# Optimization experiments

Measured on AMD Instinct MI355X. Metric: run time of the kernel, lower is better.

Reference implementation:

```python
import jax, jax.numpy as jnp
import numpy as np

N, S, F, D = 4096, 128, 128, 256  # batch, memory slots, feat_dim, dim_h_o
EPS = 1e-8  # torch CosineSimilarity eps


def _xavier(key, shape):
    fan_out, fan_in = shape
    std = float(np.sqrt(2.0 / (fan_in + fan_out)))
    return jax.random.normal(key, shape, dtype=jnp.float32) * std


def setup_inputs() -> dict:
    key = jax.random.key(0)
    ks = jax.random.split(key, 10)
    return {
        "h_o_prev": jax.random.normal(ks[0], (N, D), dtype=jnp.float32),
        "C": jax.random.normal(ks[1], (N, S, F), dtype=jnp.float32),
        "Wk": _xavier(ks[2], (F, D)), "bk": jnp.zeros((F,), jnp.float32),
        "Wb": _xavier(ks[3], (1, D)), "bb": jnp.zeros((1,), jnp.float32),
        "We": _xavier(ks[4], (F, D)), "be": jnp.zeros((F,), jnp.float32),
        "Wv": _xavier(ks[5], (F, D)), "bv": jnp.zeros((F,), jnp.float32),
        "Wih": _xavier(ks[6], (3 * D, F)), "Whh": _xavier(ks[7], (3 * D, D)),
        "bih": jnp.zeros((3 * D,), jnp.float32), "bhh": jnp.zeros((3 * D,), jnp.float32),
    }


def reference(h_o_prev, C, Wk, bk, Wb, bb, We, be, Wv, bv, Wih, Whh, bih, bhh):
    # --- Attention (content addressing) ---
    k = h_o_prev @ Wk.T + bk                              # [N, F]
    beta_pre = h_o_prev @ Wb.T + bb                       # [N, 1]
    # clamp-split softplus trick in source == softplus(x) + 1
    beta = jax.nn.softplus(beta_pre) + 1.0                # [N, 1]
    C_norm = jnp.maximum(jnp.linalg.norm(C, axis=2), EPS)           # [N, S]
    k_norm = jnp.maximum(jnp.linalg.norm(k, axis=1, keepdims=True), EPS)  # [N, 1]
    s = jnp.einsum("nsf,nf->ns", C, k) / (C_norm * k_norm)          # cosine sim [N, S]
    w = jax.nn.softmax(s * beta, axis=1)                  # [N, S]
    # --- Read memory ---
    r = jnp.einsum("ns,nsf->nf", w, C)                    # [N, F]
    # --- GRU cell update (torch GRUCell semantics) ---
    gi = r @ Wih.T + bih                                  # [N, 3D]
    gh = h_o_prev @ Whh.T + bhh                           # [N, 3D]
    i_r, i_z, i_n = jnp.split(gi, 3, axis=1)
    h_r, h_z, h_n = jnp.split(gh, 3, axis=1)
    rg = jax.nn.sigmoid(i_r + h_r)
    z = jax.nn.sigmoid(i_z + h_z)
    n = jnp.tanh(i_n + rg * h_n)
    h_o = (1.0 - z) * n + z * h_o_prev                    # [N, D]
    # --- Write memory (erase + add, outer products) ---
    e = jax.nn.sigmoid(h_o @ We.T + be)                   # [N, F]
    v = h_o @ Wv.T + bv                                   # [N, F]
    w2 = w[:, :, None]                                    # [N, S, 1]
    C_new = C * (1.0 - w2 * e[:, None, :]) + w2 * v[:, None, :]
    return h_o, C_new, k, r
```

## Files before the change

kernel.cpp:

```cpp
#include <hip/hip_runtime.h>
#include <hip/hip_bf16.h>
#include <cstddef>
#include <cstdint>

constexpr int Nn = 4096;
constexpr int Ss = 128;
constexpr int Ff = 128;
constexpr int Dd = 256;
constexpr float EPSV = 1e-8f;

constexpr size_t HO_OFF = 0;
constexpr size_t C_OFF  = (size_t)Nn * Dd;
constexpr size_t K_OFF  = C_OFF + (size_t)Nn * Ss * Ff;
constexpr size_t R_OFF  = K_OFF + (size_t)Nn * Ff;

typedef __attribute__((ext_vector_type(4))) float f4v;
typedef __attribute__((ext_vector_type(8))) short bh8;

__device__ __forceinline__ float sigmf(float x) { return 1.0f / (1.0f + __expf(-x)); }

__device__ __forceinline__ short f2bf(float x) {
    __hip_bfloat16 h = __float2bfloat16(x);
    return *reinterpret_cast<short*>(&h);
}

template <int SIGSPLIT>
__global__ __launch_bounds__(256) void mfma_gemm(
    const float* __restrict__ A, int K,
    const float* __restrict__ W1, const float* __restrict__ W2, int splitW,
    const float* __restrict__ b1, const float* __restrict__ b2,
    float* __restrict__ out1, int J1,
    float* __restrict__ out2, int J2, int splitOut)
{
    __shared__ __align__(16) short sA[64 * 32];
    __shared__ __align__(16) short sW[64 * 32];

    const int t  = threadIdx.x;
    const int bm = blockIdx.x * 64;
    const int bj = blockIdx.y * 64;

    const int r  = t >> 2;
    const int kg = t & 3;
    const float* aRow = A + (size_t)(bm + r) * K;
    const int   colS  = bj + r;
    const float* wRow = (colS < splitW) ? (W1 + (size_t)colS * K)
                                        : (W2 + (size_t)(colS - splitW) * K);
    const int swzSt = r * 32 + ((kg ^ (r & 3)) << 3);

    const int l   = t & 63;
    const int wv  = t >> 6;
    const int wr  = wv >> 1;
    const int wc  = wv & 1;
    const int kgr = l >> 4;
    const int fr  = l & 15;

    f4v acc[2][2];
#pragma unroll
    for (int m = 0; m < 2; ++m)
#pragma unroll
        for (int n2 = 0; n2 < 2; ++n2) acc[m][n2] = f4v{0.f, 0.f, 0.f, 0.f};

    const int nk = K / 32;
    for (int kc = 0; kc < nk; ++kc) {
        const int k0 = kc * 32 + kg * 8;
        float4 a0 = *(const float4*)(aRow + k0);
        float4 a1 = *(const float4*)(aRow + k0 + 4);
        float4 w0 = *(const float4*)(wRow + k0);
        float4 w1 = *(const float4*)(wRow + k0 + 4);
        bh8 av = { f2bf(a0.x), f2bf(a0.y), f2bf(a0.z), f2bf(a0.w),
                   f2bf(a1.x), f2bf(a1.y), f2bf(a1.z), f2bf(a1.w) };
        bh8 wvv= { f2bf(w0.x), f2bf(w0.y), f2bf(w0.z), f2bf(w0.w),
                   f2bf(w1.x), f2bf(w1.y), f2bf(w1.z), f2bf(w1.w) };
        __syncthreads();
        *(bh8*)(sA + swzSt) = av;
        *(bh8*)(sW + swzSt) = wvv;
        __syncthreads();

        bh8 af[2], bf[2];
#pragma unroll
        for (int m = 0; m < 2; ++m) {
            int ar = wr * 32 + m * 16 + fr;
            af[m] = *(bh8*)(sA + ar * 32 + ((kgr ^ (ar & 3)) << 3));
            int bc = wc * 32 + m * 16 + fr;
            bf[m] = *(bh8*)(sW + bc * 32 + ((kgr ^ (bc & 3)) << 3));
        }
#pragma unroll
        for (int m = 0; m < 2; ++m)
#pragma unroll
            for (int n2 = 0; n2 < 2; ++n2)
                acc[m][n2] = __builtin_amdgcn_mfma_f32_16x16x32_bf16(
                    af[m], bf[n2], acc[m][n2], 0, 0, 0);
    }

#pragma unroll
    for (int n2 = 0; n2 < 2; ++n2) {
        const int colg = bj + wc * 32 + n2 * 16 + fr;
        const float bs = (colg < splitW) ? b1[colg] : b2[colg - splitW];
        float* base; int jj;
        if (colg < splitOut) { base = out1 + colg;              jj = J1; }
        else                 { base = out2 + (colg - splitOut); jj = J2; }
#pragma unroll
        for (int m = 0; m < 2; ++m) {
#pragma unroll
            for (int rg = 0; rg < 4; ++rg) {
                float x = acc[m][n2][rg] + bs;
                if (SIGSPLIT && colg < SIGSPLIT) x = sigmf(x);
                const int rowg = bm + wr * 32 + m * 16 + kgr * 4 + rg;
                base[(size_t)rowg * jj] = x;
            }
        }
    }
}

__global__ __launch_bounds__(256) void beta_kernel(
    const float* __restrict__ h, const float* __restrict__ Wb,
    const float* __restrict__ bb, float* __restrict__ beta_out)
{
    int wid  = threadIdx.x >> 6;
    int lane = threadIdx.x & 63;
    int n    = blockIdx.x * 4 + wid;
    float4 hv = *(const float4*)(h + (size_t)n * Dd + lane * 4);
    float4 wv = *(const float4*)(Wb + lane * 4);
    float p = hv.x * wv.x + hv.y * wv.y + hv.z * wv.z + hv.w * wv.w;
#pragma unroll
    for (int o = 32; o > 0; o >>= 1) p += __shfl_xor(p, o);
    if (lane == 0) {
        float bp = p + bb[0];
        float sp = (bp > 20.0f) ? bp : log1pf(__expf(bp));
        beta_out[n] = sp + 1.0f;
    }
}

__global__ __launch_bounds__(256) void attn_kernel(
    const float* __restrict__ C, const float* __restrict__ kvec,
    const float* __restrict__ beta_arr,
    float* __restrict__ w_out, float* __restrict__ r_out)
{
    const int n    = blockIdx.x;
    const int t    = threadIdx.x;
    const int lane = t & 63;
    const int wid  = t >> 6;
    const float* Cn = C + (size_t)n * Ss * Ff;

    __shared__ float sk[Ff];
    __shared__ float ssc[Ss];
    __shared__ float sred[8];
    __shared__ float sw[Ss];
    __shared__ float sr4[8][Ff];

    if (t < Ff) sk[t] = kvec[(size_t)n * Ff + t];
    __syncthreads();

    float ks = 0.0f;
    if (t < Ff) { float kv = sk[t]; ks = kv * kv; }
#pragma unroll
    for (int o = 32; o > 0; o >>= 1) ks += __shfl_xor(ks, o);
    if (lane == 0) sred[wid] = ks;
    __syncthreads();
    const float knorm = fmaxf(sqrtf(sred[0] + sred[1]), EPSV);
    const float beta  = beta_arr[n];

#pragma unroll 4
    for (int it = 0; it < 16; ++it) {
        int s = wid * 32 + it * 2 + (lane >> 5);
        int f = (lane & 31) * 4;
        float4 c4 = *(const float4*)(Cn + (size_t)s * Ff + f);
        float d = c4.x * sk[f] + c4.y * sk[f + 1] + c4.z * sk[f + 2] + c4.w * sk[f + 3];
        float q = c4.x * c4.x + c4.y * c4.y + c4.z * c4.z + c4.w * c4.w;
#pragma unroll
        for (int o = 16; o > 0; o >>= 1) {
            d += __shfl_xor(d, o);
            q += __shfl_xor(q, o);
        }
        if ((lane & 31) == 0) {
            float cn = fmaxf(sqrtf(q), EPSV);
            ssc[s] = d / (cn * knorm);
        }
    }
    __syncthreads();

    float x = -INFINITY;
    if (t < Ss) x = ssc[t] * beta;
    float m = x;
#pragma unroll
    for (int o = 32; o > 0; o >>= 1) m = fmaxf(m, __shfl_xor(m, o));
    if (lane == 0) sred[wid] = m;
    __syncthreads();
    const float gm = fmaxf(sred[0], sred[1]);
    float ex = (t < Ss) ? __expf(x - gm) : 0.0f;
    float sm = ex;
#pragma unroll
    for (int o = 32; o > 0; o >>= 1) sm += __shfl_xor(sm, o);
    if (lane == 0) sred[4 + wid] = sm;
    __syncthreads();
    const float tot = sred[4] + sred[5];
    if (t < Ss) {
        float wvl = ex / tot;
        sw[t] = wvl;
        w_out[(size_t)n * Ss + t] = wvl;
    }
    __syncthreads();

    const int f4 = (t & 31) * 4;
    const int sg = t >> 5;
    float4 racc = make_float4(0.f, 0.f, 0.f, 0.f);
#pragma unroll 4
    for (int j = 0; j < 16; ++j) {
        int s = sg * 16 + j;
        float wvl = sw[s];
        float4 c4 = *(const float4*)(Cn + (size_t)s * Ff + f4);
        racc.x += wvl * c4.x;
        racc.y += wvl * c4.y;
        racc.z += wvl * c4.z;
        racc.w += wvl * c4.w;
    }
    *(float4*)(&sr4[sg][f4]) = racc;
    __syncthreads();
    if (t < 32) {
        float4 rr = *(float4*)(&sr4[0][t * 4]);
#pragma unroll
        for (int g = 1; g < 8; ++g) {
            float4 p = *(float4*)(&sr4[g][t * 4]);
            rr.x += p.x; rr.y += p.y; rr.z += p.z; rr.w += p.w;
        }
        *(float4*)(r_out + (size_t)n * Ff + t * 4) = rr;
    }
}

__global__ __launch_bounds__(256) void gates_kernel(
    const float* __restrict__ gi, const float* __restrict__ gh,
    const float* __restrict__ hprev, float* __restrict__ ho)
{
    int idx = blockIdx.x * blockDim.x + threadIdx.x;
    int n  = idx >> 6;
    int d4 = (idx & 63) * 4;
    const float* gin = gi + (size_t)n * 768;
    const float* ghn = gh + (size_t)n * 768;
    float4 ir = *(const float4*)(gin + d4);
    float4 iz = *(const float4*)(gin + 256 + d4);
    float4 in_ = *(const float4*)(gin + 512 + d4);
    float4 hr = *(const float4*)(ghn + d4);
    float4 hz = *(const float4*)(ghn + 256 + d4);
    float4 hn = *(const float4*)(ghn + 512 + d4);
    float4 hp = *(const float4*)(hprev + (size_t)n * Dd + d4);
    float4 o;
    { float rg = sigmf(ir.x + hr.x); float z = sigmf(iz.x + hz.x);
      float nn = tanhf(in_.x + rg * hn.x); o.x = (1.0f - z) * nn + z * hp.x; }
    { float rg = sigmf(ir.y + hr.y); float z = sigmf(iz.y + hz.y);
      float nn = tanhf(in_.y + rg * hn.y); o.y = (1.0f - z) * nn + z * hp.y; }
    { float rg = sigmf(ir.z + hr.z); float z = sigmf(iz.z + hz.z);
      float nn = tanhf(in_.z + rg * hn.z); o.z = (1.0f - z) * nn + z * hp.z; }
    { float rg = sigmf(ir.w + hr.w); float z = sigmf(iz.w + hz.w);
      float nn = tanhf(in_.w + rg * hn.w); o.w = (1.0f - z) * nn + z * hp.w; }
    *(float4*)(ho + (size_t)n * Dd + d4) = o;
}

__global__ __launch_bounds__(256) void update_kernel(
    const float* __restrict__ C, const float* __restrict__ w,
    const float* __restrict__ ev, float* __restrict__ Cnew)
{
    const size_t total4 = (size_t)Nn * Ss * Ff / 4;
    const size_t stride = (size_t)gridDim.x * blockDim.x;
    const size_t lin    = (size_t)blockIdx.x * blockDim.x + threadIdx.x;
    const int nIter     = (int)(total4 / stride);
    for (int it = nIter - 1; it >= 0; --it) {
        size_t i = (size_t)it * stride + lin;
        int n   = (int)(i >> 12);
        int rem = (int)(i & 4095);
        int s   = rem >> 5;
        int f4  = (rem & 31) * 4;
        float wv = w[(size_t)n * Ss + s];
        float4 e4 = *(const float4*)(ev + (size_t)n * 256 + f4);
        float4 v4 = *(const float4*)(ev + (size_t)n * 256 + 128 + f4);
        f4v c4 = __builtin_nontemporal_load((const f4v*)(C + i * 4));
        f4v o;
        o.x = c4.x * (1.0f - wv * e4.x) + wv * v4.x;
        o.y = c4.y * (1.0f - wv * e4.y) + wv * v4.y;
        o.z = c4.z * (1.0f - wv * e4.z) + wv * v4.z;
        o.w = c4.w * (1.0f - wv * e4.w) + wv * v4.w;
        __builtin_nontemporal_store(o, (f4v*)(Cnew + i * 4));
    }
}

extern "C" void kernel_launch(void* const* d_in, const int* in_sizes, int n_in,
                              void* d_out, int out_size, void* d_ws, size_t ws_size,
                              hipStream_t stream)
{
    const float* h_prev = (const float*)d_in[0];
    const float* C      = (const float*)d_in[1];
    const float* Wk     = (const float*)d_in[2];
    const float* bk     = (const float*)d_in[3];
    const float* Wb     = (const float*)d_in[4];
    const float* bb     = (const float*)d_in[5];
    const float* We     = (const float*)d_in[6];
    const float* be     = (const float*)d_in[7];
    const float* Wv     = (const float*)d_in[8];
    const float* bv     = (const float*)d_in[9];
    const float* Wih    = (const float*)d_in[10];
    const float* Whh    = (const float*)d_in[11];
    const float* bih    = (const float*)d_in[12];
    const float* bhh    = (const float*)d_in[13];

    float* out  = (float*)d_out;
    float* ho   = out + HO_OFF;
    float* Cnew = out + C_OFF;
    float* kbuf = out + K_OFF;
    float* rbuf = out + R_OFF;

    float* ws      = (float*)d_ws;
    float* ws_gh   = ws;
    float* ws_gi   = ws_gh + (size_t)Nn * 768;
    float* ws_beta = ws_gi + (size_t)Nn * 768;
    float* ws_w    = ws_beta + Nn;
    float* ws_ev   = ws_w + (size_t)Nn * Ss;

    mfma_gemm<0><<<dim3(Nn / 64, 896 / 64), 256, 0, stream>>>(
        h_prev, Dd, Whh, Wk, 768, bhh, bk, ws_gh, 768, kbuf, 128, 768);

    beta_kernel<<<Nn / 4, 256, 0, stream>>>(h_prev, Wb, bb, ws_beta);

    attn_kernel<<<Nn, 256, 0, stream>>>(C, kbuf, ws_beta, ws_w, rbuf);

    mfma_gemm<0><<<dim3(Nn / 64, 768 / 64), 256, 0, stream>>>(
        rbuf, Ff, Wih, Wih, 768, bih, bih, ws_gi, 768, nullptr, 0, 768);

    gates_kernel<<<(Nn * Dd / 4) / 256, 256, 0, stream>>>(ws_gi, ws_gh, h_prev, ho);

    mfma_gemm<128><<<dim3(Nn / 64, 256 / 64), 256, 0, stream>>>(
        ho, Dd, We, Wv, 128, be, bv, ws_ev, 256, nullptr, 0, 256);

    update_kernel<<<8192, 256, 0, stream>>>(C, ws_w, ws_ev, Cnew);
}
```

Measured before the change: 227.8 us.

## Fuse key/beta projections into attention, cache C in LDS as bf16, batch GRU GEMMs

The k projection and the beta softplus are now computed inside the attention kernel, one block per row, each thread dotting a Wk row against h in shared memory. This removes the separate beta kernel and the k round-trip through global memory. The attention kernel also stores C as bf16 in LDS so the weighted read pass no longer re-reads C from global memory, at the cost of bf16 rounding in r and higher LDS use that may lower occupancy. The h·Whh and r·Wih GEMMs are merged into one launch using a z-dimension, and the GEMM loops register-prefetch the next K tile.

```diff
diff --git a/kernel.cpp b/kernel.cpp
--- a/kernel.cpp
+++ b/kernel.cpp
@@ -16,6 +16,7 @@
 
 typedef __attribute__((ext_vector_type(4))) float f4v;
 typedef __attribute__((ext_vector_type(8))) short bh8;
+typedef __attribute__((ext_vector_type(4))) short bh4;
 
 __device__ __forceinline__ float sigmf(float x) { return 1.0f / (1.0f + __expf(-x)); }
 
@@ -23,17 +24,23 @@
     __hip_bfloat16 h = __float2bfloat16(x);
     return *reinterpret_cast<short*>(&h);
 }
-
-template <int SIGSPLIT>
-__global__ __launch_bounds__(256) void mfma_gemm(
-    const float* __restrict__ A, int K,
-    const float* __restrict__ W1, const float* __restrict__ W2, int splitW,
-    const float* __restrict__ b1, const float* __restrict__ b2,
-    float* __restrict__ out1, int J1,
-    float* __restrict__ out2, int J2, int splitOut)
+__device__ __forceinline__ float bf2f(short s) {
+    return __uint_as_float(((unsigned int)(unsigned short)s) << 16);
+}
+
+
+__global__ __launch_bounds__(256) void gemm_dual(
+    const float* __restrict__ A0, int K0, const float* __restrict__ W0,
+    const float* __restrict__ bias0, float* __restrict__ out0,
+    const float* __restrict__ A1, int K1, const float* __restrict__ W1,
+    const float* __restrict__ bias1, float* __restrict__ out1, int J)
 {
     __shared__ __align__(16) short sA[64 * 32];
     __shared__ __align__(16) short sW[64 * 32];
+
+    const float* A;  const float* W;  const float* bias;  float* out;  int K;
+    if (blockIdx.z == 0) { A = A0; W = W0; bias = bias0; out = out0; K = K0; }
+    else                 { A = A1; W = W1; bias = bias1; out = out1; K = K1; }
 
     const int t  = threadIdx.x;
     const int bm = blockIdx.x * 64;
@@ -42,9 +49,7 @@
     const int r  = t >> 2;
     const int kg = t & 3;
     const float* aRow = A + (size_t)(bm + r) * K;
-    const int   colS  = bj + r;
-    const float* wRow = (colS < splitW) ? (W1 + (size_t)colS * K)
-                                        : (W2 + (size_t)(colS - splitW) * K);
+    const float* wRow = W + (size_t)(bj + r) * K;
     const int swzSt = r * 32 + ((kg ^ (r & 3)) << 3);
 
     const int l   = t & 63;
@@ -61,21 +66,27 @@
         for (int n2 = 0; n2 < 2; ++n2) acc[m][n2] = f4v{0.f, 0.f, 0.f, 0.f};
 
     const int nk = K / 32;
+    float4 a0 = *(const float4*)(aRow + kg * 8);
+    float4 a1 = *(const float4*)(aRow + kg * 8 + 4);
+    float4 w0 = *(const float4*)(wRow + kg * 8);
+    float4 w1 = *(const float4*)(wRow + kg * 8 + 4);
+
     for (int kc = 0; kc < nk; ++kc) {
-        const int k0 = kc * 32 + kg * 8;
-        float4 a0 = *(const float4*)(aRow + k0);
-        float4 a1 = *(const float4*)(aRow + k0 + 4);
-        float4 w0 = *(const float4*)(wRow + k0);
-        float4 w1 = *(const float4*)(wRow + k0 + 4);
         bh8 av = { f2bf(a0.x), f2bf(a0.y), f2bf(a0.z), f2bf(a0.w),
                    f2bf(a1.x), f2bf(a1.y), f2bf(a1.z), f2bf(a1.w) };
-        bh8 wvv= { f2bf(w0.x), f2bf(w0.y), f2bf(w0.z), f2bf(w0.w),
+        bh8 wv8= { f2bf(w0.x), f2bf(w0.y), f2bf(w0.z), f2bf(w0.w),
                    f2bf(w1.x), f2bf(w1.y), f2bf(w1.z), f2bf(w1.w) };
         __syncthreads();
         *(bh8*)(sA + swzSt) = av;
-        *(bh8*)(sW + swzSt) = wvv;
+        *(bh8*)(sW + swzSt) = wv8;
         __syncthreads();
-
+        if (kc + 1 < nk) {
+            const int k0 = (kc + 1) * 32 + kg * 8;
+            a0 = *(const float4*)(aRow + k0);
+            a1 = *(const float4*)(aRow + k0 + 4);
+            w0 = *(const float4*)(wRow + k0);
+            w1 = *(const float4*)(wRow + k0 + 4);
+        }
         bh8 af[2], bf[2];
 #pragma unroll
         for (int m = 0; m < 2; ++m) {
@@ -95,46 +106,111 @@
 #pragma unroll
     for (int n2 = 0; n2 < 2; ++n2) {
         const int colg = bj + wc * 32 + n2 * 16 + fr;
-        const float bs = (colg < splitW) ? b1[colg] : b2[colg - splitW];
-        float* base; int jj;
-        if (colg < splitOut) { base = out1 + colg;              jj = J1; }
-        else                 { base = out2 + (colg - splitOut); jj = J2; }
+        const float bs = bias[colg];
+#pragma unroll
+        for (int m = 0; m < 2; ++m)
+#pragma unroll
+            for (int rg = 0; rg < 4; ++rg) {
+                const int rowg = bm + wr * 32 + m * 16 + kgr * 4 + rg;
+                out[(size_t)rowg * J + colg] = acc[m][n2][rg] + bs;
+            }
+    }
+}
+
+__global__ __launch_bounds__(256) void gemm_ev(
+    const float* __restrict__ A,
+    const float* __restrict__ We, const float* __restrict__ Wv,
+    const float* __restrict__ be, const float* __restrict__ bv,
+    float* __restrict__ out)
+{
+    constexpr int K = 256, J = 256;
+    __shared__ __align__(16) short sA[64 * 32];
+    __shared__ __align__(16) short sW[64 * 32];
+
+    const int t  = threadIdx.x;
+    const int bm = blockIdx.x * 64;
+    const int bj = blockIdx.y * 64;
+
+    const int r  = t >> 2;
+    const int kg = t & 3;
+    const float* aRow = A + (size_t)(bm + r) * K;
+    const int colS = bj + r;
+    const float* wRow = (colS < 128) ? (We + (size_t)colS * K)
+                                     : (Wv + (size_t)(colS - 128) * K);
+    const int swzSt = r * 32 + ((kg ^ (r & 3)) << 3);
+
+    const int l   = t & 63;
+    const int wv  = t >> 6;
+    const int wr  = wv >> 1;
+    const int wc  = wv & 1;
+    const int kgr = l >> 4;
+    const int fr  = l & 15;
+
+    f4v acc[2][2];
+#pragma unroll
+    for (int m = 0; m < 2; ++m)
+#pragma unroll
+        for (int n2 = 0; n2 < 2; ++n2) acc[m][n2] = f4v{0.f, 0.f, 0.f, 0.f};
+
+    const int nk = K / 32;
+    float4 a0 = *(const float4*)(aRow + kg * 8);
+    float4 a1 = *(const float4*)(aRow + kg * 8 + 4);
+    float4 w0 = *(const float4*)(wRow + kg * 8);
+    float4 w1 = *(const float4*)(wRow + kg * 8 + 4);
+
+    for (int kc = 0; kc < nk; ++kc) {
+        bh8 av = { f2bf(a0.x), f2bf(a0.y), f2bf(a0.z), f2bf(a0.w),
+                   f2bf(a1.x), f2bf(a1.y), f2bf(a1.z), f2bf(a1.w) };
+        bh8 wv8= { f2bf(w0.x), f2bf(w0.y), f2bf(w0.z), f2bf(w0.w),
+                   f2bf(w1.x), f2bf(w1.y), f2bf(w1.z), f2bf(w1.w) };
+        __syncthreads();
+        *(bh8*)(sA + swzSt) = av;
+        *(bh8*)(sW + swzSt) = wv8;
+        __syncthreads();
+        if (kc + 1 < nk) {
+            const int k0 = (kc + 1) * 32 + kg * 8;
+            a0 = *(const float4*)(aRow + k0);
+            a1 = *(const float4*)(aRow + k0 + 4);
+            w0 = *(const float4*)(wRow + k0);
+            w1 = *(const float4*)(wRow + k0 + 4);
+        }
+        bh8 af[2], bf[2];
 #pragma unroll
         for (int m = 0; m < 2; ++m) {
+            int ar = wr * 32 + m * 16 + fr;
+            af[m] = *(bh8*)(sA + ar * 32 + ((kgr ^ (ar & 3)) << 3));
+            int bc = wc * 32 + m * 16 + fr;
+            bf[m] = *(bh8*)(sW + bc * 32 + ((kgr ^ (bc & 3)) << 3));
+        }
+#pragma unroll
+        for (int m = 0; m < 2; ++m)
+#pragma unroll
+            for (int n2 = 0; n2 < 2; ++n2)
+                acc[m][n2] = __builtin_amdgcn_mfma_f32_16x16x32_bf16(
+                    af[m], bf[n2], acc[m][n2], 0, 0, 0);
+    }
+
+#pragma unroll
+    for (int n2 = 0; n2 < 2; ++n2) {
+        const int colg = bj + wc * 32 + n2 * 16 + fr;
+        const float bs = (colg < 128) ? be[colg] : bv[colg - 128];
+#pragma unroll
+        for (int m = 0; m < 2; ++m)
 #pragma unroll
             for (int rg = 0; rg < 4; ++rg) {
                 float x = acc[m][n2][rg] + bs;
-                if (SIGSPLIT && colg < SIGSPLIT) x = sigmf(x);
+                if (colg < 128) x = sigmf(x);
                 const int rowg = bm + wr * 32 + m * 16 + kgr * 4 + rg;
-                base[(size_t)rowg * jj] = x;
+                out[(size_t)rowg * J + colg] = x;
             }
-        }
-    }
-}
-
-__global__ __launch_bounds__(256) void beta_kernel(
-    const float* __restrict__ h, const float* __restrict__ Wb,
-    const float* __restrict__ bb, float* __restrict__ beta_out)
-{
-    int wid  = threadIdx.x >> 6;
-    int lane = threadIdx.x & 63;
-    int n    = blockIdx.x * 4 + wid;
-    float4 hv = *(const float4*)(h + (size_t)n * Dd + lane * 4);
-    float4 wv = *(const float4*)(Wb + lane * 4);
-    float p = hv.x * wv.x + hv.y * wv.y + hv.z * wv.z + hv.w * wv.w;
-#pragma unroll
-    for (int o = 32; o > 0; o >>= 1) p += __shfl_xor(p, o);
-    if (lane == 0) {
-        float bp = p + bb[0];
-        float sp = (bp > 20.0f) ? bp : log1pf(__expf(bp));
-        beta_out[n] = sp + 1.0f;
     }
 }
 
 __global__ __launch_bounds__(256) void attn_kernel(
-    const float* __restrict__ C, const float* __restrict__ kvec,
-    const float* __restrict__ beta_arr,
-    float* __restrict__ w_out, float* __restrict__ r_out)
+    const float* __restrict__ C, const float* __restrict__ h_prev,
+    const float* __restrict__ Wk, const float* __restrict__ bk,
+    const float* __restrict__ Wb, const float* __restrict__ bb,
+    float* __restrict__ k_out, float* __restrict__ w_out, float* __restrict__ r_out)
 {
     const int n    = blockIdx.x;
     const int t    = threadIdx.x;
@@ -142,29 +218,64 @@
     const int wid  = t >> 6;
     const float* Cn = C + (size_t)n * Ss * Ff;
 
+    __shared__ float sH[Dd];
     __shared__ float sk[Ff];
+    __shared__ __align__(16) short sC[Ss * Ff];
     __shared__ float ssc[Ss];
-    __shared__ float sred[8];
     __shared__ float sw[Ss];
+    __shared__ float sred[16];
     __shared__ float sr4[8][Ff];
 
-    if (t < Ff) sk[t] = kvec[(size_t)n * Ff + t];
-    __syncthreads();
-
-    float ks = 0.0f;
-    if (t < Ff) { float kv = sk[t]; ks = kv * kv; }
-#pragma unroll
-    for (int o = 32; o > 0; o >>= 1) ks += __shfl_xor(ks, o);
-    if (lane == 0) sred[wid] = ks;
+    sH[t] = h_prev[(size_t)n * Dd + t];
+    __syncthreads();
+
+    {
+        const int j = t >> 1, half = t & 1;
+        const float* wr = Wk + (size_t)j * Dd + half * 128;
+        const float* hh = sH + half * 128;
+        float acc = 0.0f;
+#pragma unroll 8
+        for (int d4 = 0; d4 < 128; d4 += 4) {
+            float4 wv = *(const float4*)(wr + d4);
+            float4 hv = *(const float4*)(hh + d4);
+            acc += wv.x * hv.x + wv.y * hv.y + wv.z * hv.z + wv.w * hv.w;
+        }
+        acc += __shfl_xor(acc, 1);
+        if (half == 0) {
+            float kv = acc + bk[j];
+            sk[j] = kv;
+            k_out[(size_t)n * Ff + j] = kv;
+        }
+    }
+    if (t < 64) {
+        float4 hv = *(const float4*)(sH + t * 4);
+        float4 wv = *(const float4*)(Wb + t * 4);
+        float p = hv.x * wv.x + hv.y * wv.y + hv.z * wv.z + hv.w * wv.w;
+#pragma unroll
+        for (int o = 32; o > 0; o >>= 1) p += __shfl_xor(p, o);
+        if (t == 0) sred[8] = p;
+    }
+    __syncthreads();
+
+    if (t < Ss) {
+        float kv = sk[t];
+        float ks = kv * kv;
+#pragma unroll
+        for (int o = 32; o > 0; o >>= 1) ks += __shfl_xor(ks, o);
+        if (lane == 0) sred[wid] = ks;
+    }
     __syncthreads();
     const float knorm = fmaxf(sqrtf(sred[0] + sred[1]), EPSV);
-    const float beta  = beta_arr[n];
+    float bp = sred[8] + bb[0];
+    const float beta = ((bp > 20.0f) ? bp : log1pf(__expf(bp))) + 1.0f;
 
 #pragma unroll 4
     for (int it = 0; it < 16; ++it) {
         int s = wid * 32 + it * 2 + (lane >> 5);
         int f = (lane & 31) * 4;
         float4 c4 = *(const float4*)(Cn + (size_t)s * Ff + f);
+        bh4 cb = { f2bf(c4.x), f2bf(c4.y), f2bf(c4.z), f2bf(c4.w) };
+        *(bh4*)(sC + s * Ff + f) = cb;
         float d = c4.x * sk[f] + c4.y * sk[f + 1] + c4.z * sk[f + 2] + c4.w * sk[f + 3];
         float q = c4.x * c4.x + c4.y * c4.y + c4.z * c4.z + c4.w * c4.w;
 #pragma unroll
@@ -208,11 +319,11 @@
     for (int j = 0; j < 16; ++j) {
         int s = sg * 16 + j;
         float wvl = sw[s];
-        float4 c4 = *(const float4*)(Cn + (size_t)s * Ff + f4);
-        racc.x += wvl * c4.x;
-        racc.y += wvl * c4.y;
-        racc.z += wvl * c4.z;
-        racc.w += wvl * c4.w;
+        bh4 cb = *(const bh4*)(sC + s * Ff + f4);
+        racc.x += wvl * bf2f(cb.x);
+        racc.y += wvl * bf2f(cb.y);
+        racc.z += wvl * bf2f(cb.z);
+        racc.w += wvl * bf2f(cb.w);
     }
     *(float4*)(&sr4[sg][f4]) = racc;
     __syncthreads();
@@ -307,27 +418,22 @@
     float* kbuf = out + K_OFF;
     float* rbuf = out + R_OFF;
 
-    float* ws      = (float*)d_ws;
-    float* ws_gh   = ws;
-    float* ws_gi   = ws_gh + (size_t)Nn * 768;
-    float* ws_beta = ws_gi + (size_t)Nn * 768;
-    float* ws_w    = ws_beta + Nn;
-    float* ws_ev   = ws_w + (size_t)Nn * Ss;
-
-    mfma_gemm<0><<<dim3(Nn / 64, 896 / 64), 256, 0, stream>>>(
-        h_prev, Dd, Whh, Wk, 768, bhh, bk, ws_gh, 768, kbuf, 128, 768);
-
-    beta_kernel<<<Nn / 4, 256, 0, stream>>>(h_prev, Wb, bb, ws_beta);
-
-    attn_kernel<<<Nn, 256, 0, stream>>>(C, kbuf, ws_beta, ws_w, rbuf);
-
-    mfma_gemm<0><<<dim3(Nn / 64, 768 / 64), 256, 0, stream>>>(
-        rbuf, Ff, Wih, Wih, 768, bih, bih, ws_gi, 768, nullptr, 0, 768);
+    float* ws    = (float*)d_ws;
+    float* ws_gh = ws;
+    float* ws_gi = ws_gh + (size_t)Nn * 768;
+    float* ws_w  = ws_gi + (size_t)Nn * 768;
+    float* ws_ev = ws_w + (size_t)Nn * Ss;
+
+    attn_kernel<<<Nn, 256, 0, stream>>>(C, h_prev, Wk, bk, Wb, bb,
+                                        kbuf, ws_w, rbuf);
+
+    gemm_dual<<<dim3(Nn / 64, 768 / 64, 2), 256, 0, stream>>>(
+        h_prev, Dd, Whh, bhh, ws_gh,
+        rbuf,   Ff, Wih, bih, ws_gi, 768);
 
     gates_kernel<<<(Nn * Dd / 4) / 256, 256, 0, stream>>>(ws_gi, ws_gh, h_prev, ho);
 
-    mfma_gemm<128><<<dim3(Nn / 64, 256 / 64), 256, 0, stream>>>(
-        ho, Dd, We, Wv, 128, be, bv, ws_ev, 256, nullptr, 0, 256);
+    gemm_ev<<<dim3(Nn / 64, 256 / 64), 256, 0, stream>>>(ho, We, Wv, be, bv, ws_ev);
 
     update_kernel<<<8192, 256, 0, stream>>>(C, ws_w, ws_ev, Cnew);
 }
```

Result: slower. 237.9 us (+4.4%).
